# Performance work log

Measured on AMD Instinct MI355X. Metric: run time of the kernel, lower is better.

The kernel has to match this reference:

```python
import jax, jax.numpy as jnp
import numpy as np

N_NODES = 200000
N_EDGES = 3200000
N_GRAPHS = 4096
IN_CH = 78
H1, H2, OUT_DIM = 64, 128, 128


def setup_inputs() -> dict:
    key = jax.random.key(0)
    ks = jax.random.split(key, 10)
    x = jax.random.normal(ks[0], (N_NODES, IN_CH), dtype=jnp.float32)
    edge_index = jax.random.randint(ks[1], (2, N_EDGES), 0, N_NODES, dtype=jnp.int64)
    batch = jnp.sort(jax.random.randint(ks[2], (N_NODES,), 0, N_GRAPHS, dtype=jnp.int64))
    # GCNConv weights (PyG: lin has no bias by default; conv bias added after aggregation)
    def glorot(k, fan_in, fan_out):
        lim = jnp.sqrt(6.0 / (fan_in + fan_out)).astype(jnp.float32)
        return jax.random.uniform(k, (fan_in, fan_out), jnp.float32, -lim, lim)
    W1 = glorot(ks[3], IN_CH, H1)
    b1 = jnp.zeros((H1,), jnp.float32)
    W2 = glorot(ks[4], H1, H2)
    b2 = jnp.zeros((H2,), jnp.float32)
    fc_w = glorot(ks[5], H2, OUT_DIM)
    fc_b = jnp.zeros((OUT_DIM,), jnp.float32)
    return {"x": x, "edge_index": edge_index, "batch": batch,
            "W1": W1, "b1": b1, "W2": W2, "b2": b2, "fc_w": fc_w, "fc_b": fc_b}


def _gcn_forward(x, edge_index, batch, W1, b1, W2, b2, fc_w, fc_b):
    N = x.shape[0]
    # GCNConv default: add self loops, symmetric deg^-1/2 normalization
    self_loops = jnp.arange(N, dtype=edge_index.dtype)
    src = jnp.concatenate([edge_index[0], self_loops])  # [E+N]
    dst = jnp.concatenate([edge_index[1], self_loops])  # [E+N]
    deg = jax.ops.segment_sum(jnp.ones_like(dst, dtype=jnp.float32), dst,
                              num_segments=N)  # in-degree incl self loop
    dinv = jnp.where(deg > 0, jax.lax.rsqrt(jnp.maximum(deg, 1.0)), 0.0)
    norm = dinv[src] * dinv[dst]  # [E+N]

    def gcn_layer(h, W, b):
        hw = h @ W                              # transform first (small dims)
        msg = hw[src] * norm[:, None]           # gather + scale  [E+N, F]
        agg = jax.ops.segment_sum(msg, dst, num_segments=N)  # scatter-add
        return agg + b

    h = jax.nn.relu(gcn_layer(x, W1, b1))
    h = jax.nn.relu(gcn_layer(h, W2, b2))
    # global_mean_pool over per-graph segments
    counts = jax.ops.segment_sum(jnp.ones((N,), jnp.float32), batch,
                                 num_segments=N_GRAPHS)
    pooled = jax.ops.segment_sum(h, batch, num_segments=N_GRAPHS)
    pooled = pooled / jnp.maximum(counts, 1.0)[:, None]  # [G, H2]
    return pooled @ fc_w + fc_b                           # [G, OUT_DIM]


def reference(x, edge_index, batch, W1, b1, W2, b2, fc_w, fc_b):
    return _gcn_forward(x, edge_index, batch, W1, b1, W2, b2, fc_w, fc_b)
```

## Files before the change

kernel.cpp:

```cpp
#include <hip/hip_runtime.h>
#include <hip/hip_bf16.h>

#define NN 200000
#define NE 3200000
#define NG 4096
#define INC 78
#define C1 64
#define C2 128
#define ODIM 128
#define KP1 96

#define BSZ 256
#define NBKT 782
#define NBLK 392
#define EPB 8164
#define CAP 8192

using bf16 = __hip_bfloat16;
typedef __attribute__((ext_vector_type(8))) short bf16x8;
typedef __attribute__((ext_vector_type(4))) float f32x4;

static inline size_t alignup(size_t x) { return (x + 255) & ~size_t(255); }

__device__ __forceinline__ float bflo(unsigned u) { return __uint_as_float(u << 16); }
__device__ __forceinline__ float bfhi(unsigned u) { return __uint_as_float(u & 0xffff0000u); }
__device__ __forceinline__ unsigned short f2bf(float f) {
    __hip_bfloat16 h = __float2bfloat16(f);
    return *reinterpret_cast<unsigned short*>(&h);
}

__global__ __launch_bounds__(256) void binsort_kernel(const int* __restrict__ src,
                                                      const int* __restrict__ dst,
                                                      int* __restrict__ gcursor,
                                                      unsigned* __restrict__ ebuf) {
    __shared__ unsigned recs[EPB + 28];
    __shared__ unsigned short bkts[EPB + 28];
    __shared__ int lh[NBKT];
    for (int j = threadIdx.x; j < NBKT; j += 256) lh[j] = 0;
    __syncthreads();
    int e0 = blockIdx.x * EPB;
    int e1 = e0 + EPB; if (e1 > NE) e1 = NE;
    int n = e1 - e0;
    for (int i = threadIdx.x; i < n; i += 256) {
        int d = dst[e0 + i];
        int s = src[e0 + i];
        recs[i] = ((unsigned)s << 8) | (unsigned)(d & 255);
        int b = ((unsigned)d) >> 8;
        bkts[i] = (unsigned short)b;
        atomicAdd(&lh[b], 1);
    }
    __syncthreads();
    for (int j = threadIdx.x; j < NBKT; j += 256) {
        int c = lh[j];
        lh[j] = (c > 0) ? atomicAdd(&gcursor[j], c) : 0;
    }
    __syncthreads();
    for (int i = threadIdx.x; i < n; i += 256) {
        int b = bkts[i];
        int off = atomicAdd(&lh[b], 1);
        if (off < CAP) ebuf[(size_t)b * CAP + off] = recs[i];
    }
}

__global__ void bucketscan_kernel(const int* __restrict__ gcursor, int* __restrict__ bstart) {
    __shared__ int tmp[1024];
    int tid = threadIdx.x;
    int v = (tid < NBKT) ? gcursor[tid] : 0;
    tmp[tid] = v;
    __syncthreads();
    for (int off = 1; off < 1024; off <<= 1) {
        int t = (tid >= off) ? tmp[tid - off] : 0;
        __syncthreads();
        tmp[tid] += t;
        __syncthreads();
    }
    if (tid < NBKT) bstart[tid] = tmp[tid] - v;
    if (tid == NBKT) bstart[NBKT] = NE;
}

__global__ __launch_bounds__(256) void degcsr_kernel(
    const unsigned* __restrict__ ebuf, const int* __restrict__ gcursor,
    const int* __restrict__ bstart, int* __restrict__ rs, float* __restrict__ dinv,
    unsigned* __restrict__ csr) {
    __shared__ int cnt[BSZ];
    __shared__ int pfx[BSZ];
    __shared__ unsigned recs[CAP];
    int b = blockIdx.x;
    int nrec = gcursor[b]; if (nrec > CAP) nrec = CAP;
    int s0 = bstart[b];
    cnt[threadIdx.x] = 0;
    for (int i = threadIdx.x; i < nrec; i += 256) recs[i] = ebuf[(size_t)b * CAP + i];
    __syncthreads();
    for (int i = threadIdx.x; i < nrec; i += 256)
        atomicAdd(&cnt[recs[i] & 255], 1);
    __syncthreads();
    int v = cnt[threadIdx.x];
    pfx[threadIdx.x] = v;
    __syncthreads();
    for (int off = 1; off < 256; off <<= 1) {
        int t = (threadIdx.x >= off) ? pfx[threadIdx.x - off] : 0;
        __syncthreads();
        pfx[threadIdx.x] += t;
        __syncthreads();
    }
    int myrs = s0 + pfx[threadIdx.x] - v;
    int node = b * BSZ + threadIdx.x;
    if (node < NN) {
        rs[node] = myrs;
        dinv[node] = rsqrtf((float)v + 1.0f);
    }
    if (node == NN) rs[NN] = NE;
    __syncthreads();
    cnt[threadIdx.x] = 0;
    pfx[threadIdx.x] = myrs;
    __syncthreads();
    for (int i = threadIdx.x; i < nrec; i += 256) {
        unsigned rec = recs[i];
        int nl = rec & 255;
        int pos = atomicAdd(&cnt[nl], 1);
        csr[pfx[nl] + pos] = rec >> 8;
    }
}

__global__ void convw2_kernel(const float* __restrict__ W1, const float* __restrict__ W2,
                              unsigned short* __restrict__ Wt1, unsigned short* __restrict__ Wt2) {
    int idx = blockIdx.x * 256 + threadIdx.x;
    if (idx < C1 * KP1) {
        int c = idx / KP1, k = idx % KP1;
        Wt1[idx] = f2bf((k < INC) ? W1[k * C1 + c] : 0.f);
    } else {
        int j = idx - C1 * KP1;
        if (j < C2 * C1) {
            int c = j / C1, k = j % C1;
            Wt2[j] = f2bf(W2[k * C2 + c]);
        }
    }
}

__global__ __launch_bounds__(256) void gemm1_mfma(const float* __restrict__ x,
                                                  const unsigned short* __restrict__ Wt1,
                                                  const float* __restrict__ dinv,
                                                  unsigned short* __restrict__ hw1s) {
    __shared__ float xs[64 * INC];
    const float4* gsrc = (const float4*)(x + (size_t)blockIdx.x * 64 * INC);
    float4* ldst = (float4*)xs;
    #pragma unroll
    for (int t = 0; t < 5; ++t) {
        int i = t * 256 + threadIdx.x;
        if (i < (64 * INC) / 4) ldst[i] = gsrc[i];
    }
    __syncthreads();
    int wave = threadIdx.x >> 6, lane = threadIdx.x & 63;
    int r = lane & 15, kg = lane >> 4;
    int lrow = wave * 16 + r;
    int row0 = blockIdx.x * 64 + wave * 16;
    const float* arow = xs + lrow * INC;
    bf16x8 a[3];
    #pragma unroll
    for (int t = 0; t < 3; ++t) {
        union { bf16x8 v; unsigned short u[8]; } tmp;
        #pragma unroll
        for (int j = 0; j < 8; ++j) {
            int k = t * 32 + kg * 8 + j;
            tmp.u[j] = (k < INC) ? f2bf(arow[k]) : (unsigned short)0;
        }
        a[t] = tmp.v;
    }
    float dsc[4];
    #pragma unroll
    for (int i = 0; i < 4; ++i) dsc[i] = dinv[row0 + kg * 4 + i];
    #pragma unroll
    for (int nt = 0; nt < 4; ++nt) {
        const unsigned short* wrow = Wt1 + (size_t)(nt * 16 + r) * KP1 + kg * 8;
        bf16x8 b0 = *(const bf16x8*)(wrow);
        bf16x8 b1 = *(const bf16x8*)(wrow + 32);
        bf16x8 b2 = *(const bf16x8*)(wrow + 64);
        f32x4 acc = {0.f, 0.f, 0.f, 0.f};
        acc = __builtin_amdgcn_mfma_f32_16x16x32_bf16(a[0], b0, acc, 0, 0, 0);
        acc = __builtin_amdgcn_mfma_f32_16x16x32_bf16(a[1], b1, acc, 0, 0, 0);
        acc = __builtin_amdgcn_mfma_f32_16x16x32_bf16(a[2], b2, acc, 0, 0, 0);
        unsigned short* cb = hw1s + (size_t)(row0 + kg * 4) * C1 + nt * 16 + r;
        #pragma unroll
        for (int i = 0; i < 4; ++i) cb[(size_t)i * C1] = f2bf(acc[i] * dsc[i]);
    }
}

__device__ __forceinline__ void gather_node(
    const unsigned* __restrict__ csr, int start, int len,
    const unsigned short* __restrict__ vin, int c0,
    float& a0, float& a1, float& a2, float& a3,
    float& a4, float& a5, float& a6, float& a7) {
    int e = 0;
    for (; e + 4 <= len; e += 4) {
        unsigned s0 = csr[start + e + 0];
        unsigned s1 = csr[start + e + 1];
        unsigned s2 = csr[start + e + 2];
        unsigned s3 = csr[start + e + 3];
        uint4 r0 = *(const uint4*)(vin + (size_t)s0 * 64 + c0);
        uint4 r1 = *(const uint4*)(vin + (size_t)s1 * 64 + c0);
        uint4 r2 = *(const uint4*)(vin + (size_t)s2 * 64 + c0);
        uint4 r3 = *(const uint4*)(vin + (size_t)s3 * 64 + c0);
        a0 += (bflo(r0.x) + bflo(r1.x)) + (bflo(r2.x) + bflo(r3.x));
        a1 += (bfhi(r0.x) + bfhi(r1.x)) + (bfhi(r2.x) + bfhi(r3.x));
        a2 += (bflo(r0.y) + bflo(r1.y)) + (bflo(r2.y) + bflo(r3.y));
        a3 += (bfhi(r0.y) + bfhi(r1.y)) + (bfhi(r2.y) + bfhi(r3.y));
        a4 += (bflo(r0.z) + bflo(r1.z)) + (bflo(r2.z) + bflo(r3.z));
        a5 += (bfhi(r0.z) + bfhi(r1.z)) + (bfhi(r2.z) + bfhi(r3.z));
        a6 += (bflo(r0.w) + bflo(r1.w)) + (bflo(r2.w) + bflo(r3.w));
        a7 += (bfhi(r0.w) + bfhi(r1.w)) + (bfhi(r2.w) + bfhi(r3.w));
    }
    for (; e < len; ++e) {
        unsigned s = csr[start + e];
        uint4 ra = *(const uint4*)(vin + (size_t)s * 64 + c0);
        a0 += bflo(ra.x); a1 += bfhi(ra.x);
        a2 += bflo(ra.y); a3 += bfhi(ra.y);
        a4 += bflo(ra.z); a5 += bfhi(ra.z);
        a6 += bflo(ra.w); a7 += bfhi(ra.w);
    }
}

template <int EP>
__global__ __launch_bounds__(256) void agg_csr_kernel(
    const unsigned* __restrict__ csr, const int* __restrict__ rs,
    const float* __restrict__ dinv, const unsigned short* __restrict__ vin,
    const float* __restrict__ bias, unsigned short* __restrict__ vout) {
    int node = blockIdx.x * 32 + (threadIdx.x >> 3);
    int l = threadIdx.x & 7;
    int c0 = l * 8;
    int start = rs[node], len = rs[node + 1] - start;
    float a0 = 0.f, a1 = 0.f, a2 = 0.f, a3 = 0.f, a4 = 0.f, a5 = 0.f, a6 = 0.f, a7 = 0.f;
    gather_node(csr, start, len, vin, c0, a0, a1, a2, a3, a4, a5, a6, a7);
    uint4 sv = *(const uint4*)(vin + (size_t)node * 64 + c0);
    a0 += bflo(sv.x); a1 += bfhi(sv.x);
    a2 += bflo(sv.y); a3 += bfhi(sv.y);
    a4 += bflo(sv.z); a5 += bfhi(sv.z);
    a6 += bflo(sv.w); a7 += bfhi(sv.w);
    float d = dinv[node];
    if (EP == 1) {
        a0 = fmaxf(a0 * d + bias[c0 + 0], 0.f) * d;
        a1 = fmaxf(a1 * d + bias[c0 + 1], 0.f) * d;
        a2 = fmaxf(a2 * d + bias[c0 + 2], 0.f) * d;
        a3 = fmaxf(a3 * d + bias[c0 + 3], 0.f) * d;
        a4 = fmaxf(a4 * d + bias[c0 + 4], 0.f) * d;
        a5 = fmaxf(a5 * d + bias[c0 + 5], 0.f) * d;
        a6 = fmaxf(a6 * d + bias[c0 + 6], 0.f) * d;
        a7 = fmaxf(a7 * d + bias[c0 + 7], 0.f) * d;
    } else {
        a0 *= d; a1 *= d; a2 *= d; a3 *= d; a4 *= d; a5 *= d; a6 *= d; a7 *= d;
    }
    uint4 o;
    o.x = (unsigned)f2bf(a0) | ((unsigned)f2bf(a1) << 16);
    o.y = (unsigned)f2bf(a2) | ((unsigned)f2bf(a3) << 16);
    o.z = (unsigned)f2bf(a4) | ((unsigned)f2bf(a5) << 16);
    o.w = (unsigned)f2bf(a6) | ((unsigned)f2bf(a7) << 16);
    *(uint4*)(vout + (size_t)node * 64 + c0) = o;
}

__global__ __launch_bounds__(256) void gemm2_mfma(const unsigned short* __restrict__ aggH,
                                                  const unsigned short* __restrict__ Wt2,
                                                  const float* __restrict__ b2,
                                                  unsigned short* __restrict__ h2) {
    int wave = threadIdx.x >> 6, lane = threadIdx.x & 63;
    int r = lane & 15, kg = lane >> 4;
    int row0 = blockIdx.x * 64 + wave * 16;
    const unsigned short* arow = aggH + (size_t)(row0 + r) * 64 + kg * 8;
    bf16x8 a0 = *(const bf16x8*)(arow);
    bf16x8 a1 = *(const bf16x8*)(arow + 32);
    #pragma unroll
    for (int nt = 0; nt < 8; ++nt) {
        const unsigned short* wrow = Wt2 + (size_t)(nt * 16 + r) * C1 + kg * 8;
        bf16x8 b0 = *(const bf16x8*)(wrow);
        bf16x8 b1 = *(const bf16x8*)(wrow + 32);
        f32x4 acc = {0.f, 0.f, 0.f, 0.f};
        acc = __builtin_amdgcn_mfma_f32_16x16x32_bf16(a0, b0, acc, 0, 0, 0);
        acc = __builtin_amdgcn_mfma_f32_16x16x32_bf16(a1, b1, acc, 0, 0, 0);
        int col = nt * 16 + r;
        float bb = b2[col];
        unsigned short* cb = h2 + (size_t)(row0 + kg * 4) * C2 + col;
        #pragma unroll
        for (int i = 0; i < 4; ++i) cb[(size_t)i * C2] = f2bf(fmaxf(acc[i] + bb, 0.f));
    }
}

__device__ __forceinline__ int lbound(const int* __restrict__ a, int n, int key) {
    int lo = 0, hi = n;
    while (lo < hi) {
        int mid = (lo + hi) >> 1;
        if (a[mid] < key) lo = mid + 1; else hi = mid;
    }
    return lo;
}

__global__ __launch_bounds__(256) void pool_fc_kernel(const unsigned short* __restrict__ h2,
                                                      const int* __restrict__ batch,
                                                      const float* __restrict__ fcw,
                                                      const float* __restrict__ fcb,
                                                      float* __restrict__ out) {
    __shared__ float ps[512];
    __shared__ float pr[128];
    int g = blockIdx.x;
    int lo = lbound(batch, NN, g);
    int hi = lbound(batch, NN, g + 1);
    int cnt = hi - lo;
    int rg = threadIdx.x >> 6;
    int p = threadIdx.x & 63;
    float s0 = 0.f, s1 = 0.f;
    for (int r = lo + rg; r < hi; r += 4) {
        unsigned v = *(const unsigned*)(h2 + (size_t)r * C2 + p * 2);
        s0 += bflo(v);
        s1 += bfhi(v);
    }
    ps[threadIdx.x * 2 + 0] = s0;
    ps[threadIdx.x * 2 + 1] = s1;
    __syncthreads();
    if (threadIdx.x < 64) {
        float inv = 1.0f / (float)((cnt > 0) ? cnt : 1);
        int t = threadIdx.x;
        float r0 = 0.f, r1 = 0.f;
        #pragma unroll
        for (int k = 0; k < 4; ++k) {
            r0 += ps[(k * 64 + t) * 2 + 0];
            r1 += ps[(k * 64 + t) * 2 + 1];
        }
        pr[2 * t + 0] = r0 * inv;
        pr[2 * t + 1] = r1 * inv;
    }
    __syncthreads();
    if (threadIdx.x < 128) {
        int o = threadIdx.x;
        float acc = fcb[o];
        #pragma unroll 8
        for (int k = 0; k < C2; ++k) acc += pr[k] * fcw[k * ODIM + o];
        out[(size_t)g * ODIM + o] = acc;
    }
}

extern "C" void kernel_launch(void* const* d_in, const int* in_sizes, int n_in,
                              void* d_out, int out_size, void* d_ws, size_t ws_size,
                              hipStream_t stream) {
    const float* x   = (const float*)d_in[0];
    const int*   ei  = (const int*)d_in[1];
    const int*   bat = (const int*)d_in[2];
    const float* W1  = (const float*)d_in[3];
    const float* b1  = (const float*)d_in[4];
    const float* W2  = (const float*)d_in[5];
    const float* b2  = (const float*)d_in[6];
    const float* fcw = (const float*)d_in[7];
    const float* fcb = (const float*)d_in[8];
    float* out = (float*)d_out;

    const int* src = ei;
    const int* dst = ei + NE;

    char* ws = (char*)d_ws;
    int* gcursor = (int*)ws;            ws += alignup((size_t)NBKT * 4);
    int* bstart  = (int*)ws;            ws += alignup((size_t)(NBKT + 1) * 4);
    int* rs      = (int*)ws;            ws += alignup((size_t)(NN + 1) * 4);
    float* dinv  = (float*)ws;          ws += alignup((size_t)NN * 4);
    unsigned short* Wt1 = (unsigned short*)ws;  ws += alignup((size_t)C1 * KP1 * 2);
    unsigned short* Wt2 = (unsigned short*)ws;  ws += alignup((size_t)C2 * C1 * 2);
    unsigned short* hw1s = (unsigned short*)ws; ws += alignup((size_t)NN * C1 * 2);
    unsigned short* aggH = hw1s;
    unsigned* ebuf = (unsigned*)ws;     ws += alignup((size_t)NBKT * CAP * 4);
    unsigned* csr  = (unsigned*)ws;     ws += alignup((size_t)NE * 4);
    unsigned short* h1s = (unsigned short*)ws;  ws += alignup((size_t)NN * C1 * 2);
    unsigned short* h2 = (unsigned short*)ebuf;

    hipMemsetAsync(gcursor, 0, (size_t)NBKT * 4, stream);
    binsort_kernel<<<NBLK, 256, 0, stream>>>(src, dst, gcursor, ebuf);
    bucketscan_kernel<<<1, 1024, 0, stream>>>(gcursor, bstart);

    degcsr_kernel<<<NBKT, 256, 0, stream>>>(ebuf, gcursor, bstart, rs, dinv, csr);

    convw2_kernel<<<(C1 * KP1 + C2 * C1 + 255) / 256, 256, 0, stream>>>(W1, W2, Wt1, Wt2);

    gemm1_mfma<<<NN / 64, 256, 0, stream>>>(x, Wt1, dinv, hw1s);
    agg_csr_kernel<1><<<NN / 32, 256, 0, stream>>>(csr, rs, dinv, hw1s, b1, h1s);

    agg_csr_kernel<2><<<NN / 32, 256, 0, stream>>>(csr, rs, dinv, h1s, b1, aggH);
    gemm2_mfma<<<NN / 64, 256, 0, stream>>>(aggH, Wt2, b2, h2);

    pool_fc_kernel<<<NG, 256, 0, stream>>>(h2, bat, fcw, fcb, out);
}
```

Baseline: 288.4 us.

## Remove bucketscan and weight-conversion kernels by fusing their work into consumers

Drops the separate bucket prefix-scan kernel: each degcsr block now rescans the global bucket counts itself to find its start offset. Drops the weight transpose/convert kernel: gemm1 and gemm2 now stage the fp32 weights in padded shared memory and convert them to bf16 per block. binsort no longer buffers records in shared memory and instead rereads src and dst from global. The aim is fewer kernel launches and less shared memory, at the cost of redundant per-block weight staging, repeated scans and extra global reads.

Result: no change. 288.2 us (-0.1%).

```diff
diff --git a/kernel.cpp b/kernel.cpp
--- a/kernel.cpp
+++ b/kernel.cpp
@@ -8,7 +8,6 @@
 #define C1 64
 #define C2 128
 #define ODIM 128
-#define KP1 96
 
 #define BSZ 256
 #define NBKT 782
@@ -33,88 +32,87 @@
                                                       const int* __restrict__ dst,
                                                       int* __restrict__ gcursor,
                                                       unsigned* __restrict__ ebuf) {
-    __shared__ unsigned recs[EPB + 28];
-    __shared__ unsigned short bkts[EPB + 28];
     __shared__ int lh[NBKT];
     for (int j = threadIdx.x; j < NBKT; j += 256) lh[j] = 0;
     __syncthreads();
     int e0 = blockIdx.x * EPB;
     int e1 = e0 + EPB; if (e1 > NE) e1 = NE;
-    int n = e1 - e0;
-    for (int i = threadIdx.x; i < n; i += 256) {
-        int d = dst[e0 + i];
-        int s = src[e0 + i];
-        recs[i] = ((unsigned)s << 8) | (unsigned)(d & 255);
-        int b = ((unsigned)d) >> 8;
-        bkts[i] = (unsigned short)b;
-        atomicAdd(&lh[b], 1);
-    }
+    for (int e = e0 + threadIdx.x; e < e1; e += 256)
+        atomicAdd(&lh[((unsigned)dst[e]) >> 8], 1);
     __syncthreads();
     for (int j = threadIdx.x; j < NBKT; j += 256) {
         int c = lh[j];
         lh[j] = (c > 0) ? atomicAdd(&gcursor[j], c) : 0;
     }
     __syncthreads();
-    for (int i = threadIdx.x; i < n; i += 256) {
-        int b = bkts[i];
+    for (int e = e0 + threadIdx.x; e < e1; e += 256) {
+        int d = dst[e];
+        int s = src[e];
+        int b = ((unsigned)d) >> 8;
         int off = atomicAdd(&lh[b], 1);
-        if (off < CAP) ebuf[(size_t)b * CAP + off] = recs[i];
-    }
-}
-
-__global__ void bucketscan_kernel(const int* __restrict__ gcursor, int* __restrict__ bstart) {
-    __shared__ int tmp[1024];
-    int tid = threadIdx.x;
-    int v = (tid < NBKT) ? gcursor[tid] : 0;
-    tmp[tid] = v;
-    __syncthreads();
-    for (int off = 1; off < 1024; off <<= 1) {
-        int t = (tid >= off) ? tmp[tid - off] : 0;
-        __syncthreads();
-        tmp[tid] += t;
-        __syncthreads();
-    }
-    if (tid < NBKT) bstart[tid] = tmp[tid] - v;
-    if (tid == NBKT) bstart[NBKT] = NE;
+        if (off < CAP) ebuf[(size_t)b * CAP + off] = ((unsigned)s << 8) | (unsigned)(d & 255);
+    }
 }
 
 __global__ __launch_bounds__(256) void degcsr_kernel(
     const unsigned* __restrict__ ebuf, const int* __restrict__ gcursor,
-    const int* __restrict__ bstart, int* __restrict__ rs, float* __restrict__ dinv,
-    unsigned* __restrict__ csr) {
+    int* __restrict__ rs, float* __restrict__ dinv, unsigned* __restrict__ csr) {
     __shared__ int cnt[BSZ];
     __shared__ int pfx[BSZ];
+    __shared__ int seg[BSZ];
+    __shared__ int gc[NBKT];
     __shared__ unsigned recs[CAP];
+    __shared__ int s0_sh;
     int b = blockIdx.x;
-    int nrec = gcursor[b]; if (nrec > CAP) nrec = CAP;
-    int s0 = bstart[b];
-    cnt[threadIdx.x] = 0;
-    for (int i = threadIdx.x; i < nrec; i += 256) recs[i] = ebuf[(size_t)b * CAP + i];
-    __syncthreads();
-    for (int i = threadIdx.x; i < nrec; i += 256)
+    int t = threadIdx.x;
+    for (int j = t; j < NBKT; j += 256) gc[j] = gcursor[j];
+    __syncthreads();
+    int ssum = 0;
+    #pragma unroll
+    for (int k = 0; k < 4; ++k) { int j = t * 4 + k; if (j < NBKT) ssum += gc[j]; }
+    seg[t] = ssum;
+    __syncthreads();
+    for (int off = 1; off < 256; off <<= 1) {
+        int v = (t >= off) ? seg[t - off] : 0;
+        __syncthreads();
+        seg[t] += v;
+        __syncthreads();
+    }
+    if (t == 0) {
+        int tb = b >> 2;
+        int ex = (tb > 0) ? seg[tb - 1] : 0;
+        for (int j = tb * 4; j < b; ++j) ex += gc[j];
+        s0_sh = ex;
+    }
+    int nrec = gc[b]; if (nrec > CAP) nrec = CAP;
+    cnt[t] = 0;
+    for (int i = t; i < nrec; i += 256) recs[i] = ebuf[(size_t)b * CAP + i];
+    __syncthreads();
+    int s0 = s0_sh;
+    for (int i = t; i < nrec; i += 256)
         atomicAdd(&cnt[recs[i] & 255], 1);
     __syncthreads();
-    int v = cnt[threadIdx.x];
-    pfx[threadIdx.x] = v;
+    int v = cnt[t];
+    pfx[t] = v;
     __syncthreads();
     for (int off = 1; off < 256; off <<= 1) {
-        int t = (threadIdx.x >= off) ? pfx[threadIdx.x - off] : 0;
+        int u = (t >= off) ? pfx[t - off] : 0;
         __syncthreads();
-        pfx[threadIdx.x] += t;
+        pfx[t] += u;
         __syncthreads();
     }
-    int myrs = s0 + pfx[threadIdx.x] - v;
-    int node = b * BSZ + threadIdx.x;
+    int myrs = s0 + pfx[t] - v;
+    int node = b * BSZ + t;
     if (node < NN) {
         rs[node] = myrs;
         dinv[node] = rsqrtf((float)v + 1.0f);
     }
     if (node == NN) rs[NN] = NE;
     __syncthreads();
-    cnt[threadIdx.x] = 0;
-    pfx[threadIdx.x] = myrs;
-    __syncthreads();
-    for (int i = threadIdx.x; i < nrec; i += 256) {
+    cnt[t] = 0;
+    pfx[t] = myrs;
+    __syncthreads();
+    for (int i = t; i < nrec; i += 256) {
         unsigned rec = recs[i];
         int nl = rec & 255;
         int pos = atomicAdd(&cnt[nl], 1);
@@ -122,39 +120,29 @@
     }
 }
 
-__global__ void convw2_kernel(const float* __restrict__ W1, const float* __restrict__ W2,
-                              unsigned short* __restrict__ Wt1, unsigned short* __restrict__ Wt2) {
-    int idx = blockIdx.x * 256 + threadIdx.x;
-    if (idx < C1 * KP1) {
-        int c = idx / KP1, k = idx % KP1;
-        Wt1[idx] = f2bf((k < INC) ? W1[k * C1 + c] : 0.f);
-    } else {
-        int j = idx - C1 * KP1;
-        if (j < C2 * C1) {
-            int c = j / C1, k = j % C1;
-            Wt2[j] = f2bf(W2[k * C2 + c]);
-        }
-    }
-}
-
 __global__ __launch_bounds__(256) void gemm1_mfma(const float* __restrict__ x,
-                                                  const unsigned short* __restrict__ Wt1,
+                                                  const float* __restrict__ W1,
                                                   const float* __restrict__ dinv,
                                                   unsigned short* __restrict__ hw1s) {
-    __shared__ float xs[64 * INC];
-    const float4* gsrc = (const float4*)(x + (size_t)blockIdx.x * 64 * INC);
-    float4* ldst = (float4*)xs;
-    #pragma unroll
-    for (int t = 0; t < 5; ++t) {
-        int i = t * 256 + threadIdx.x;
-        if (i < (64 * INC) / 4) ldst[i] = gsrc[i];
+    __shared__ unsigned short xs[64 * INC];
+    __shared__ float w1s[INC * 65];
+    for (int i = threadIdx.x; i < (INC * C1) / 2; i += 256) {
+        float2 w = ((const float2*)W1)[i];
+        int k = (i * 2) / C1, c = (i * 2) % C1;
+        w1s[k * 65 + c] = w.x;
+        w1s[k * 65 + c + 1] = w.y;
+    }
+    const float2* gx = (const float2*)(x + (size_t)blockIdx.x * 64 * INC);
+    for (int i = threadIdx.x; i < (64 * INC) / 2; i += 256) {
+        float2 v = gx[i];
+        unsigned pk = (unsigned)f2bf(v.x) | ((unsigned)f2bf(v.y) << 16);
+        *(unsigned*)(xs + i * 2) = pk;
     }
     __syncthreads();
     int wave = threadIdx.x >> 6, lane = threadIdx.x & 63;
     int r = lane & 15, kg = lane >> 4;
     int lrow = wave * 16 + r;
     int row0 = blockIdx.x * 64 + wave * 16;
-    const float* arow = xs + lrow * INC;
     bf16x8 a[3];
     #pragma unroll
     for (int t = 0; t < 3; ++t) {
@@ -162,7 +150,7 @@
         #pragma unroll
         for (int j = 0; j < 8; ++j) {
             int k = t * 32 + kg * 8 + j;
-            tmp.u[j] = (k < INC) ? f2bf(arow[k]) : (unsigned short)0;
+            tmp.u[j] = (k < INC) ? xs[lrow * INC + k] : (unsigned short)0;
         }
         a[t] = tmp.v;
     }
@@ -171,15 +159,23 @@
     for (int i = 0; i < 4; ++i) dsc[i] = dinv[row0 + kg * 4 + i];
     #pragma unroll
     for (int nt = 0; nt < 4; ++nt) {
-        const unsigned short* wrow = Wt1 + (size_t)(nt * 16 + r) * KP1 + kg * 8;
-        bf16x8 b0 = *(const bf16x8*)(wrow);
-        bf16x8 b1 = *(const bf16x8*)(wrow + 32);
-        bf16x8 b2 = *(const bf16x8*)(wrow + 64);
+        int c = nt * 16 + r;
+        bf16x8 bf[3];
+        #pragma unroll
+        for (int t = 0; t < 3; ++t) {
+            union { bf16x8 v; unsigned short u[8]; } tb;
+            #pragma unroll
+            for (int j = 0; j < 8; ++j) {
+                int k = t * 32 + kg * 8 + j;
+                tb.u[j] = (k < INC) ? f2bf(w1s[k * 65 + c]) : (unsigned short)0;
+            }
+            bf[t] = tb.v;
+        }
         f32x4 acc = {0.f, 0.f, 0.f, 0.f};
-        acc = __builtin_amdgcn_mfma_f32_16x16x32_bf16(a[0], b0, acc, 0, 0, 0);
-        acc = __builtin_amdgcn_mfma_f32_16x16x32_bf16(a[1], b1, acc, 0, 0, 0);
-        acc = __builtin_amdgcn_mfma_f32_16x16x32_bf16(a[2], b2, acc, 0, 0, 0);
-        unsigned short* cb = hw1s + (size_t)(row0 + kg * 4) * C1 + nt * 16 + r;
+        acc = __builtin_amdgcn_mfma_f32_16x16x32_bf16(a[0], bf[0], acc, 0, 0, 0);
+        acc = __builtin_amdgcn_mfma_f32_16x16x32_bf16(a[1], bf[1], acc, 0, 0, 0);
+        acc = __builtin_amdgcn_mfma_f32_16x16x32_bf16(a[2], bf[2], acc, 0, 0, 0);
+        unsigned short* cb = hw1s + (size_t)(row0 + kg * 4) * C1 + c;
         #pragma unroll
         for (int i = 0; i < 4; ++i) cb[(size_t)i * C1] = f2bf(acc[i] * dsc[i]);
     }
@@ -257,9 +253,17 @@
 }
 
 __global__ __launch_bounds__(256) void gemm2_mfma(const unsigned short* __restrict__ aggH,
-                                                  const unsigned short* __restrict__ Wt2,
+                                                  const float* __restrict__ W2,
                                                   const float* __restrict__ b2,
                                                   unsigned short* __restrict__ h2) {
+    __shared__ float w2s[C1 * 129];
+    for (int i = threadIdx.x; i < (C1 * C2) / 2; i += 256) {
+        float2 w = ((const float2*)W2)[i];
+        int k = (i * 2) >> 7, c = (i * 2) & 127;
+        w2s[k * 129 + c] = w.x;
+        w2s[k * 129 + c + 1] = w.y;
+    }
+    __syncthreads();
     int wave = threadIdx.x >> 6, lane = threadIdx.x & 63;
     int r = lane & 15, kg = lane >> 4;
     int row0 = blockIdx.x * 64 + wave * 16;
@@ -268,13 +272,20 @@
     bf16x8 a1 = *(const bf16x8*)(arow + 32);
     #pragma unroll
     for (int nt = 0; nt < 8; ++nt) {
-        const unsigned short* wrow = Wt2 + (size_t)(nt * 16 + r) * C1 + kg * 8;
-        bf16x8 b0 = *(const bf16x8*)(wrow);
-        bf16x8 b1 = *(const bf16x8*)(wrow + 32);
+        int col = nt * 16 + r;
+        bf16x8 b0, b1;
+        {
+            union { bf16x8 v; unsigned short u[8]; } tb;
+            #pragma unroll
+            for (int j = 0; j < 8; ++j) tb.u[j] = f2bf(w2s[(kg * 8 + j) * 129 + col]);
+            b0 = tb.v;
+            #pragma unroll
+            for (int j = 0; j < 8; ++j) tb.u[j] = f2bf(w2s[(32 + kg * 8 + j) * 129 + col]);
+            b1 = tb.v;
+        }
         f32x4 acc = {0.f, 0.f, 0.f, 0.f};
         acc = __builtin_amdgcn_mfma_f32_16x16x32_bf16(a0, b0, acc, 0, 0, 0);
         acc = __builtin_amdgcn_mfma_f32_16x16x32_bf16(a1, b1, acc, 0, 0, 0);
-        int col = nt * 16 + r;
         float bb = b2[col];
         unsigned short* cb = h2 + (size_t)(row0 + kg * 4) * C2 + col;
         #pragma unroll
@@ -354,11 +365,8 @@
 
     char* ws = (char*)d_ws;
     int* gcursor = (int*)ws;            ws += alignup((size_t)NBKT * 4);
-    int* bstart  = (int*)ws;            ws += alignup((size_t)(NBKT + 1) * 4);
     int* rs      = (int*)ws;            ws += alignup((size_t)(NN + 1) * 4);
     float* dinv  = (float*)ws;          ws += alignup((size_t)NN * 4);
-    unsigned short* Wt1 = (unsigned short*)ws;  ws += alignup((size_t)C1 * KP1 * 2);
-    unsigned short* Wt2 = (unsigned short*)ws;  ws += alignup((size_t)C2 * C1 * 2);
     unsigned short* hw1s = (unsigned short*)ws; ws += alignup((size_t)NN * C1 * 2);
     unsigned short* aggH = hw1s;
     unsigned* ebuf = (unsigned*)ws;     ws += alignup((size_t)NBKT * CAP * 4);
@@ -368,17 +376,14 @@
 
     hipMemsetAsync(gcursor, 0, (size_t)NBKT * 4, stream);
     binsort_kernel<<<NBLK, 256, 0, stream>>>(src, dst, gcursor, ebuf);
-    bucketscan_kernel<<<1, 1024, 0, stream>>>(gcursor, bstart);
-
-    degcsr_kernel<<<NBKT, 256, 0, stream>>>(ebuf, gcursor, bstart, rs, dinv, csr);
-
-    convw2_kernel<<<(C1 * KP1 + C2 * C1 + 255) / 256, 256, 0, stream>>>(W1, W2, Wt1, Wt2);
-
-    gemm1_mfma<<<NN / 64, 256, 0, stream>>>(x, Wt1, dinv, hw1s);
+
+    degcsr_kernel<<<NBKT, 256, 0, stream>>>(ebuf, gcursor, rs, dinv, csr);
+
+    gemm1_mfma<<<NN / 64, 256, 0, stream>>>(x, W1, dinv, hw1s);
     agg_csr_kernel<1><<<NN / 32, 256, 0, stream>>>(csr, rs, dinv, hw1s, b1, h1s);
 
     agg_csr_kernel<2><<<NN / 32, 256, 0, stream>>>(csr, rs, dinv, h1s, b1, aggH);
-    gemm2_mfma<<<NN / 64, 256, 0, stream>>>(aggH, Wt2, b2, h2);
+    gemm2_mfma<<<NN / 64, 256, 0, stream>>>(aggH, W2, b2, h2);
 
     pool_fc_kernel<<<NG, 256, 0, stream>>>(h2, bat, fcw, fcb, out);
 }
```
